# Optimization experiments

Hardware: AMD Instinct MI355X
Metric: run time of the kernel (lower is better)

Reference implementation:

```python
import jax, jax.numpy as jnp
import numpy as np

B, T, D, F, E, TOPK = 4, 2048, 1024, 2752, 8, 2


def setup_inputs() -> dict:
    key = jax.random.key(0)
    k1, k2, k3, k4 = jax.random.split(key, 4)
    x = jax.random.normal(k1, (B, T, D), dtype=jnp.float32)
    # Expert params, torch Linear(bias=False) stored as [in, out] for x @ W
    W13 = jax.random.normal(k2, (E, D, 2 * F), dtype=jnp.float32) * 0.02  # gate+up packed
    W2 = jax.random.normal(k3, (E, F, D), dtype=jnp.float32) * 0.02       # down proj
    Wr = jax.random.normal(k4, (D, E), dtype=jnp.float32) * 0.02          # router
    return {"x": x, "W13": W13, "W2": W2, "Wr": Wr}


def reference(x, W13, W2, Wr):
    b, t, d = x.shape
    xf = x.reshape(-1, d)                       # [N, D]
    n = xf.shape[0]
    logits = xf @ Wr                            # [N, E]
    probs = jax.nn.softmax(logits, axis=-1)
    top_probs, top_idx = jax.lax.top_k(probs, TOPK)  # [N, K]
    top_probs = top_probs / top_probs.sum(axis=-1, keepdims=True)
    # combine weights: cw[n, e] = sum_k top_probs[n, k] * (top_idx[n, k] == e)
    cw = jnp.zeros((n, E), dtype=xf.dtype).at[jnp.arange(n)[:, None], top_idx].add(top_probs)
    out = jnp.zeros_like(xf)
    for e in range(E):  # small fixed expert loop; tokens with cw==0 contribute nothing
        x13 = xf @ W13[e]                       # [N, 2F]
        x1, x3 = jnp.split(x13, 2, axis=-1)
        h = jax.nn.silu(x1) * x3                # SwiGLU
        out = out + cw[:, e:e + 1] * (h @ W2[e])
    return out.reshape(b, t, d)
```

## Files before the change

kernel.cpp:

```cpp
#include <hip/hip_runtime.h>
#include <stdint.h>

#define NTOK 8192
#define DDIM 1024
#define FDIM 2752
#define NEXP 8
#define DF2  5504
#define NSLOT 16384

typedef __attribute__((ext_vector_type(8))) short bf16x8;
typedef __attribute__((ext_vector_type(4))) float f32x4;
typedef __attribute__((ext_vector_type(4))) unsigned short u16x4;
typedef __attribute__((ext_vector_type(8))) unsigned short u16x8;

constexpr size_t XB_OFF   = 0;
constexpr size_t XB_SZ    = (size_t)NTOK * DDIM * 2;
constexpr size_t W13T_OFF = XB_OFF + XB_SZ;
constexpr size_t W13T_SZ  = (size_t)NEXP * DF2 * DDIM * 2;
constexpr size_t W2T_OFF  = W13T_OFF + W13T_SZ;
constexpr size_t W2T_SZ   = (size_t)NEXP * DDIM * FDIM * 2;
constexpr size_t H_OFF    = W2T_OFF + W2T_SZ;
constexpr size_t H_SZ     = (size_t)NSLOT * FDIM * 2;
constexpr size_t ST_OFF   = H_OFF + H_SZ;
constexpr size_t SW_OFF   = ST_OFF + (size_t)NSLOT * 4;
constexpr size_t TTI_OFF  = SW_OFF + (size_t)NSLOT * 4;
constexpr size_t TTW_OFF  = TTI_OFF + (size_t)NTOK * 8;
constexpr size_t META_OFF = TTW_OFF + (size_t)NTOK * 8;

__device__ __forceinline__ unsigned short f2bf(float f) {
  unsigned u = __float_as_uint(f);
  u += 0x7FFFu + ((u >> 16) & 1u);
  return (unsigned short)(u >> 16);
}

__device__ __forceinline__ void gl_lds16(const void* g, void* l) {
  __builtin_amdgcn_global_load_lds(
      (const __attribute__((address_space(1))) unsigned int*)g,
      (__attribute__((address_space(3))) unsigned int*)l, 16, 0, 0);
}

__global__ void cvt_x_k(const float* __restrict__ x, unsigned short* __restrict__ xb) {
  int i = blockIdx.x * 256 + threadIdx.x;
  float4 v = ((const float4*)x)[i];
  u16x4 o;
  o[0] = f2bf(v.x); o[1] = f2bf(v.y); o[2] = f2bf(v.z); o[3] = f2bf(v.w);
  ((u16x4*)xb)[i] = o;
}

__global__ void tcvt_k(const float* __restrict__ src, unsigned short* __restrict__ dst,
                       int R, int C) {
  __shared__ unsigned short tile[64][65];
  long base = (long)blockIdx.z * R * C;
  src += base; dst += base;
  int r0 = blockIdx.y * 64, c0 = blockIdx.x * 64;
  int t = threadIdx.x;
  int rr = t >> 4, cc = (t & 15) * 4;
  for (int i = 0; i < 4; ++i) {
    float4 v = *(const float4*)&src[(long)(r0 + rr + i * 16) * C + c0 + cc];
    tile[rr + i * 16][cc + 0] = f2bf(v.x);
    tile[rr + i * 16][cc + 1] = f2bf(v.y);
    tile[rr + i * 16][cc + 2] = f2bf(v.z);
    tile[rr + i * 16][cc + 3] = f2bf(v.w);
  }
  __syncthreads();
  int dr = t >> 2, sg = (t & 3) * 16;
  u16x8 o0, o1;
  for (int i = 0; i < 8; ++i) { o0[i] = tile[sg + i][dr]; o1[i] = tile[sg + 8 + i][dr]; }
  unsigned short* dp = &dst[(long)(c0 + dr) * R + r0 + sg];
  *(u16x8*)dp = o0;
  *(u16x8*)(dp + 8) = o1;
}

__global__ void router_k(const float* __restrict__ x, const float* __restrict__ Wr,
                         int* __restrict__ meta, int2* __restrict__ tt_i,
                         float2* __restrict__ tt_w) {
  int lane = threadIdx.x & 63;
  int tok = blockIdx.x * 4 + (threadIdx.x >> 6);
  float acc[8];
#pragma unroll
  for (int e = 0; e < 8; ++e) acc[e] = 0.f;
  const float4* xr = (const float4*)(x + (long)tok * DDIM);
#pragma unroll
  for (int it = 0; it < 4; ++it) {
    float4 v = xr[it * 64 + lane];
    int d = (it * 64 + lane) * 4;
    float xv[4] = {v.x, v.y, v.z, v.w};
#pragma unroll
    for (int j = 0; j < 4; ++j) {
      const float4* wr = (const float4*)(Wr + (long)(d + j) * NEXP);
      float4 wa = wr[0], wb = wr[1];
      acc[0] += xv[j] * wa.x; acc[1] += xv[j] * wa.y;
      acc[2] += xv[j] * wa.z; acc[3] += xv[j] * wa.w;
      acc[4] += xv[j] * wb.x; acc[5] += xv[j] * wb.y;
      acc[6] += xv[j] * wb.z; acc[7] += xv[j] * wb.w;
    }
  }
#pragma unroll
  for (int e = 0; e < 8; ++e)
    for (int off = 32; off; off >>= 1) acc[e] += __shfl_xor(acc[e], off, 64);
  if (lane == 0) {
    float m = acc[0];
    for (int e = 1; e < 8; ++e) m = fmaxf(m, acc[e]);
    float p[8];
    for (int e = 0; e < 8; ++e) p[e] = __expf(acc[e] - m);
    int e0 = 0;
    for (int e = 1; e < 8; ++e) if (p[e] > p[e0]) e0 = e;
    int e1 = -1;
    for (int e = 0; e < 8; ++e) { if (e == e0) continue; if (e1 < 0 || p[e] > p[e1]) e1 = e; }
    float s = p[e0] + p[e1];
    atomicAdd(&meta[e0], 1);
    atomicAdd(&meta[e1], 1);
    tt_i[tok] = make_int2(e0, e1);
    tt_w[tok] = make_float2(p[e0] / s, p[e1] / s);
  }
}

__global__ void offsets_k(int* meta) {
  int run = 0;
  for (int e = 0; e < NEXP; ++e) { meta[16 + e] = run; run += meta[e]; }
}

__global__ void scatter_k(const int2* __restrict__ tt_i, const float2* __restrict__ tt_w,
                          int* __restrict__ meta, int* __restrict__ slot_tok,
                          float* __restrict__ slot_w) {
  int n = blockIdx.x * 256 + threadIdx.x;
  int2 ei = tt_i[n];
  float2 wv = tt_w[n];
  int p0 = atomicAdd(&meta[8 + ei.x], 1);
  int s0 = meta[16 + ei.x] + p0;
  slot_tok[s0] = n; slot_w[s0] = wv.x;
  int p1 = atomicAdd(&meta[8 + ei.y], 1);
  int s1 = meta[16 + ei.y] + p1;
  slot_tok[s1] = n; slot_w[s1] = wv.y;
}

__global__ __launch_bounds__(256) void gemm1_k(
    const unsigned short* __restrict__ xb, const unsigned short* __restrict__ w13t,
    const int* __restrict__ meta, const int* __restrict__ slot_tok,
    unsigned short* __restrict__ h) {
  int e = blockIdx.z;
  int n_e = meta[e];
  int m0 = blockIdx.y * 128;
  if (m0 >= n_e) return;
  int base = meta[16 + e];
  int c0 = blockIdx.x * 64;
  const unsigned short* wB = w13t + (long)e * DF2 * DDIM;

  __shared__ unsigned short Al[128 * 32];
  __shared__ unsigned short B1l[64 * 32];
  __shared__ unsigned short B2l[64 * 32];

  int t = threadIdx.x;
  int lane = t & 63, w = t >> 6;
  int wm = w & 1, wn = w >> 1;
  int ar0 = t >> 2, ac = (t & 3) * 8;

  int tokA0 = slot_tok[base + min(m0 + ar0, n_e - 1)];
  int tokA1 = slot_tok[base + min(m0 + 64 + ar0, n_e - 1)];
  const unsigned short* gA0 = xb + (long)tokA0 * DDIM + ac;
  const unsigned short* gA1 = xb + (long)tokA1 * DDIM + ac;
  const unsigned short* gB1 = wB + (long)(c0 + ar0) * DDIM + ac;
  const unsigned short* gB2 = gB1 + (long)FDIM * DDIM;

  unsigned short* lA0 = &Al[t * 8];
  unsigned short* lA1 = &Al[(t + 256) * 8];
  unsigned short* lB1 = &B1l[t * 8];
  unsigned short* lB2 = &B2l[t * 8];

  f32x4 accg[4][2], accu[4][2];
#pragma unroll
  for (int mi = 0; mi < 4; ++mi)
#pragma unroll
    for (int ni = 0; ni < 2; ++ni) {
      accg[mi][ni] = (f32x4){0.f, 0.f, 0.f, 0.f};
      accu[mi][ni] = (f32x4){0.f, 0.f, 0.f, 0.f};
    }

  for (int k0 = 0; k0 < DDIM; k0 += 32) {
    gl_lds16(gA0 + k0, lA0);
    gl_lds16(gA1 + k0, lA1);
    gl_lds16(gB1 + k0, lB1);
    gl_lds16(gB2 + k0, lB2);
    __syncthreads();
    int q8 = (lane >> 4) * 8;
    bf16x8 a[4], b1[2], b2[2];
#pragma unroll
    for (int mi = 0; mi < 4; ++mi)
      a[mi] = *(const bf16x8*)&Al[(wm * 64 + mi * 16 + (lane & 15)) * 32 + q8];
#pragma unroll
    for (int ni = 0; ni < 2; ++ni) {
      b1[ni] = *(const bf16x8*)&B1l[(wn * 32 + ni * 16 + (lane & 15)) * 32 + q8];
      b2[ni] = *(const bf16x8*)&B2l[(wn * 32 + ni * 16 + (lane & 15)) * 32 + q8];
    }
#pragma unroll
    for (int mi = 0; mi < 4; ++mi)
#pragma unroll
      for (int ni = 0; ni < 2; ++ni) {
        accg[mi][ni] = __builtin_amdgcn_mfma_f32_16x16x32_bf16(a[mi], b1[ni], accg[mi][ni], 0, 0, 0);
        accu[mi][ni] = __builtin_amdgcn_mfma_f32_16x16x32_bf16(a[mi], b2[ni], accu[mi][ni], 0, 0, 0);
      }
    __syncthreads();
  }
  int quad = lane >> 4;
  int col0 = c0 + wn * 32 + (lane & 15);
#pragma unroll
  for (int mi = 0; mi < 4; ++mi)
#pragma unroll
    for (int r = 0; r < 4; ++r) {
      int m = m0 + wm * 64 + mi * 16 + quad * 4 + r;
      if (m < n_e) {
        unsigned short* hp = &h[(long)(base + m) * FDIM + col0];
#pragma unroll
        for (int ni = 0; ni < 2; ++ni) {
          float g = accg[mi][ni][r], u = accu[mi][ni][r];
          float hv = (g / (1.f + __expf(-g))) * u;
          hp[ni * 16] = f2bf(hv);
        }
      }
    }
}

__global__ __launch_bounds__(256) void gemm2_k(
    const unsigned short* __restrict__ h, const unsigned short* __restrict__ w2t,
    const int* __restrict__ meta, const int* __restrict__ slot_tok,
    const float* __restrict__ slot_w, float* __restrict__ out) {
  int e = blockIdx.z;
  int n_e = meta[e];
  int m0 = blockIdx.y * 128;
  if (m0 >= n_e) return;
  int base = meta[16 + e];
  int n0 = blockIdx.x * 128;
  const unsigned short* wB = w2t + (long)e * DDIM * FDIM;

  __shared__ unsigned short Al[128 * 32];
  __shared__ unsigned short Bl[128 * 32];

  int t = threadIdx.x;
  int lane = t & 63, w = t >> 6;
  int wm = w & 1, wn = w >> 1;
  int ar0 = t >> 2, ac = (t & 3) * 8;

  int rA0 = base + min(m0 + ar0, n_e - 1);
  int rA1 = base + min(m0 + 64 + ar0, n_e - 1);
  const unsigned short* gA0 = h + (long)rA0 * FDIM + ac;
  const unsigned short* gA1 = h + (long)rA1 * FDIM + ac;
  const unsigned short* gB0 = wB + (long)(n0 + ar0) * FDIM + ac;
  const unsigned short* gB1 = gB0 + (long)64 * FDIM;

  unsigned short* lA0 = &Al[t * 8];
  unsigned short* lA1 = &Al[(t + 256) * 8];
  unsigned short* lB0 = &Bl[t * 8];
  unsigned short* lB1 = &Bl[(t + 256) * 8];

  f32x4 acc[4][4];
#pragma unroll
  for (int mi = 0; mi < 4; ++mi)
#pragma unroll
    for (int ni = 0; ni < 4; ++ni) acc[mi][ni] = (f32x4){0.f, 0.f, 0.f, 0.f};

  for (int k0 = 0; k0 < FDIM; k0 += 32) {
    gl_lds16(gA0 + k0, lA0);
    gl_lds16(gA1 + k0, lA1);
    gl_lds16(gB0 + k0, lB0);
    gl_lds16(gB1 + k0, lB1);
    __syncthreads();
    int q8 = (lane >> 4) * 8;
    bf16x8 a[4], b[4];
#pragma unroll
    for (int mi = 0; mi < 4; ++mi)
      a[mi] = *(const bf16x8*)&Al[(wm * 64 + mi * 16 + (lane & 15)) * 32 + q8];
#pragma unroll
    for (int ni = 0; ni < 4; ++ni)
      b[ni] = *(const bf16x8*)&Bl[(wn * 64 + ni * 16 + (lane & 15)) * 32 + q8];
#pragma unroll
    for (int mi = 0; mi < 4; ++mi)
#pragma unroll
      for (int ni = 0; ni < 4; ++ni)
        acc[mi][ni] = __builtin_amdgcn_mfma_f32_16x16x32_bf16(a[mi], b[ni], acc[mi][ni], 0, 0, 0);
    __syncthreads();
  }
  int quad = lane >> 4;
#pragma unroll
  for (int mi = 0; mi < 4; ++mi)
#pragma unroll
    for (int r = 0; r < 4; ++r) {
      int m = m0 + wm * 64 + mi * 16 + quad * 4 + r;
      if (m < n_e) {
        int tok = slot_tok[base + m];
        float wgt = slot_w[base + m];
        float* op = out + (long)tok * DDIM + n0 + wn * 64 + (lane & 15);
#pragma unroll
        for (int ni = 0; ni < 4; ++ni) atomicAdd(op + ni * 16, wgt * acc[mi][ni][r]);
      }
    }
}

extern "C" void kernel_launch(void* const* d_in, const int* in_sizes, int n_in,
                              void* d_out, int out_size, void* d_ws, size_t ws_size,
                              hipStream_t stream) {
  const float* x   = (const float*)d_in[0];
  const float* W13 = (const float*)d_in[1];
  const float* W2  = (const float*)d_in[2];
  const float* Wr  = (const float*)d_in[3];
  float* out = (float*)d_out;
  char* ws = (char*)d_ws;

  unsigned short* xb   = (unsigned short*)(ws + XB_OFF);
  unsigned short* w13t = (unsigned short*)(ws + W13T_OFF);
  unsigned short* w2t  = (unsigned short*)(ws + W2T_OFF);
  unsigned short* hbuf = (unsigned short*)(ws + H_OFF);
  int*    slot_tok = (int*)(ws + ST_OFF);
  float*  slot_w   = (float*)(ws + SW_OFF);
  int2*   tt_i     = (int2*)(ws + TTI_OFF);
  float2* tt_w     = (float2*)(ws + TTW_OFF);
  int*    meta     = (int*)(ws + META_OFF);

  hipMemsetAsync(d_out, 0, (size_t)NTOK * DDIM * sizeof(float), stream);
  hipMemsetAsync(meta, 0, 128, stream);

  cvt_x_k<<<NTOK * DDIM / 4 / 256, 256, 0, stream>>>(x, xb);
  tcvt_k<<<dim3(DF2 / 64, DDIM / 64, NEXP), 256, 0, stream>>>(W13, w13t, DDIM, DF2);
  tcvt_k<<<dim3(DDIM / 64, FDIM / 64, NEXP), 256, 0, stream>>>(W2, w2t, FDIM, DDIM);
  router_k<<<NTOK / 4, 256, 0, stream>>>(x, Wr, meta, tt_i, tt_w);
  offsets_k<<<1, 1, 0, stream>>>(meta);
  scatter_k<<<NTOK / 256, 256, 0, stream>>>(tt_i, tt_w, meta, slot_tok, slot_w);
  gemm1_k<<<dim3(FDIM / 64, NTOK / 128, NEXP), 256, 0, stream>>>(xb, w13t, meta, slot_tok, hbuf);
  gemm2_k<<<dim3(DDIM / 128, NTOK / 128, NEXP), 256, 0, stream>>>(hbuf, w2t, meta, slot_tok, slot_w, out);
}
```

Measured before the change: 1.109 ms.

## Double-buffer LDS in both expert GEMMs and replace atomic scatter with combine pass

Both grouped GEMMs now double-buffer their LDS tiles. The next K-slice is issued with global_load_lds before the current one is consumed, using explicit vmcnt waits and barriers so load latency overlaps MFMA work. The down-projection no longer atomically adds into the output. It writes weighted per-slot rows to a scratch buffer placed over the W13 workspace, and a new combine kernel sums each token's two slots. This removes atomics and the output memset, at the cost of an extra 64MB write and read pass and one more launch.

```diff
diff --git a/kernel.cpp b/kernel.cpp
--- a/kernel.cpp
+++ b/kernel.cpp
@@ -26,6 +26,7 @@
 constexpr size_t TTI_OFF  = SW_OFF + (size_t)NSLOT * 4;
 constexpr size_t TTW_OFF  = TTI_OFF + (size_t)NTOK * 8;
 constexpr size_t META_OFF = TTW_OFF + (size_t)NTOK * 8;
+constexpr size_t TS_OFF   = META_OFF + 256;
 
 __device__ __forceinline__ unsigned short f2bf(float f) {
   unsigned u = __float_as_uint(f);
@@ -38,6 +39,11 @@
       (const __attribute__((address_space(1))) unsigned int*)g,
       (__attribute__((address_space(3))) unsigned int*)l, 16, 0, 0);
 }
+
+#define WAIT_VM4 asm volatile("s_waitcnt vmcnt(4)" ::: "memory")
+#define WAIT_VM0 asm volatile("s_waitcnt vmcnt(0)" ::: "memory")
+#define WAIT_LGKM0 asm volatile("s_waitcnt lgkmcnt(0)" ::: "memory")
+#define BAR() __builtin_amdgcn_s_barrier()
 
 __global__ void cvt_x_k(const float* __restrict__ x, unsigned short* __restrict__ xb) {
   int i = blockIdx.x * 256 + threadIdx.x;
@@ -122,7 +128,7 @@
 
 __global__ void scatter_k(const int2* __restrict__ tt_i, const float2* __restrict__ tt_w,
                           int* __restrict__ meta, int* __restrict__ slot_tok,
-                          float* __restrict__ slot_w) {
+                          float* __restrict__ slot_w, int2* __restrict__ tok_slot) {
   int n = blockIdx.x * 256 + threadIdx.x;
   int2 ei = tt_i[n];
   float2 wv = tt_w[n];
@@ -132,6 +138,7 @@
   int p1 = atomicAdd(&meta[8 + ei.y], 1);
   int s1 = meta[16 + ei.y] + p1;
   slot_tok[s1] = n; slot_w[s1] = wv.y;
+  tok_slot[n] = make_int2(s0, s1);
 }
 
 __global__ __launch_bounds__(256) void gemm1_k(
@@ -146,9 +153,9 @@
   int c0 = blockIdx.x * 64;
   const unsigned short* wB = w13t + (long)e * DF2 * DDIM;
 
-  __shared__ unsigned short Al[128 * 32];
-  __shared__ unsigned short B1l[64 * 32];
-  __shared__ unsigned short B2l[64 * 32];
+  __shared__ unsigned short Al[2][128 * 32];
+  __shared__ unsigned short B1l[2][64 * 32];
+  __shared__ unsigned short B2l[2][64 * 32];
 
   int t = threadIdx.x;
   int lane = t & 63, w = t >> 6;
@@ -162,11 +169,6 @@
   const unsigned short* gB1 = wB + (long)(c0 + ar0) * DDIM + ac;
   const unsigned short* gB2 = gB1 + (long)FDIM * DDIM;
 
-  unsigned short* lA0 = &Al[t * 8];
-  unsigned short* lA1 = &Al[(t + 256) * 8];
-  unsigned short* lB1 = &B1l[t * 8];
-  unsigned short* lB2 = &B2l[t * 8];
-
   f32x4 accg[4][2], accu[4][2];
 #pragma unroll
   for (int mi = 0; mi < 4; ++mi)
@@ -176,31 +178,60 @@
       accu[mi][ni] = (f32x4){0.f, 0.f, 0.f, 0.f};
     }
 
-  for (int k0 = 0; k0 < DDIM; k0 += 32) {
-    gl_lds16(gA0 + k0, lA0);
-    gl_lds16(gA1 + k0, lA1);
-    gl_lds16(gB1 + k0, lB1);
-    gl_lds16(gB2 + k0, lB2);
-    __syncthreads();
-    int q8 = (lane >> 4) * 8;
-    bf16x8 a[4], b1[2], b2[2];
-#pragma unroll
-    for (int mi = 0; mi < 4; ++mi)
-      a[mi] = *(const bf16x8*)&Al[(wm * 64 + mi * 16 + (lane & 15)) * 32 + q8];
-#pragma unroll
-    for (int ni = 0; ni < 2; ++ni) {
-      b1[ni] = *(const bf16x8*)&B1l[(wn * 32 + ni * 16 + (lane & 15)) * 32 + q8];
-      b2[ni] = *(const bf16x8*)&B2l[(wn * 32 + ni * 16 + (lane & 15)) * 32 + q8];
-    }
-#pragma unroll
-    for (int mi = 0; mi < 4; ++mi)
-#pragma unroll
-      for (int ni = 0; ni < 2; ++ni) {
-        accg[mi][ni] = __builtin_amdgcn_mfma_f32_16x16x32_bf16(a[mi], b1[ni], accg[mi][ni], 0, 0, 0);
-        accu[mi][ni] = __builtin_amdgcn_mfma_f32_16x16x32_bf16(a[mi], b2[ni], accu[mi][ni], 0, 0, 0);
-      }
-    __syncthreads();
-  }
+  int q8 = (lane >> 4) * 8;
+  int arow = lane & 15;
+  bf16x8 a[4], b1[2], b2[2];
+
+#define G1_STAGE(bb, k0)                                      \
+  do {                                                        \
+    gl_lds16(gA0 + (k0), &Al[bb][(size_t)t * 8]);             \
+    gl_lds16(gA1 + (k0), &Al[bb][(size_t)(t + 256) * 8]);     \
+    gl_lds16(gB1 + (k0), &B1l[bb][(size_t)t * 8]);            \
+    gl_lds16(gB2 + (k0), &B2l[bb][(size_t)t * 8]);            \
+  } while (0)
+
+#define G1_FRAGS(bb)                                                          \
+  do {                                                                        \
+    const unsigned short* As = Al[bb];                                        \
+    const unsigned short* B1s = B1l[bb];                                      \
+    const unsigned short* B2s = B2l[bb];                                      \
+    _Pragma("unroll")                                                         \
+    for (int mi = 0; mi < 4; ++mi)                                            \
+      a[mi] = *(const bf16x8*)&As[(wm * 64 + mi * 16 + arow) * 32 + q8];      \
+    _Pragma("unroll")                                                         \
+    for (int ni = 0; ni < 2; ++ni) {                                          \
+      b1[ni] = *(const bf16x8*)&B1s[(wn * 32 + ni * 16 + arow) * 32 + q8];    \
+      b2[ni] = *(const bf16x8*)&B2s[(wn * 32 + ni * 16 + arow) * 32 + q8];    \
+    }                                                                         \
+  } while (0)
+
+#define G1_MFMA()                                                                                    \
+  _Pragma("unroll")                                                                                  \
+  for (int mi = 0; mi < 4; ++mi)                                                                     \
+    _Pragma("unroll")                                                                                \
+    for (int ni = 0; ni < 2; ++ni) {                                                                 \
+      accg[mi][ni] = __builtin_amdgcn_mfma_f32_16x16x32_bf16(a[mi], b1[ni], accg[mi][ni], 0, 0, 0);  \
+      accu[mi][ni] = __builtin_amdgcn_mfma_f32_16x16x32_bf16(a[mi], b2[ni], accu[mi][ni], 0, 0, 0);  \
+    }
+
+  G1_STAGE(0, 0);
+  int cur = 0;
+#pragma unroll 1
+  for (int k = 1; k < DDIM / 32; ++k) {
+    G1_STAGE(cur ^ 1, k * 32);
+    WAIT_VM4;
+    BAR();
+    G1_FRAGS(cur);
+    WAIT_LGKM0;
+    BAR();
+    G1_MFMA();
+    cur ^= 1;
+  }
+  WAIT_VM0;
+  BAR();
+  G1_FRAGS(cur);
+  G1_MFMA();
+
   int quad = lane >> 4;
   int col0 = c0 + wn * 32 + (lane & 15);
 #pragma unroll
@@ -222,8 +253,8 @@
 
 __global__ __launch_bounds__(256) void gemm2_k(
     const unsigned short* __restrict__ h, const unsigned short* __restrict__ w2t,
-    const int* __restrict__ meta, const int* __restrict__ slot_tok,
-    const float* __restrict__ slot_w, float* __restrict__ out) {
+    const int* __restrict__ meta, const float* __restrict__ slot_w,
+    float* __restrict__ y) {
   int e = blockIdx.z;
   int n_e = meta[e];
   int m0 = blockIdx.y * 128;
@@ -232,8 +263,8 @@
   int n0 = blockIdx.x * 128;
   const unsigned short* wB = w2t + (long)e * DDIM * FDIM;
 
-  __shared__ unsigned short Al[128 * 32];
-  __shared__ unsigned short Bl[128 * 32];
+  __shared__ unsigned short Al[2][128 * 32];
+  __shared__ unsigned short Bl[2][128 * 32];
 
   int t = threadIdx.x;
   int lane = t & 63, w = t >> 6;
@@ -247,38 +278,61 @@
   const unsigned short* gB0 = wB + (long)(n0 + ar0) * FDIM + ac;
   const unsigned short* gB1 = gB0 + (long)64 * FDIM;
 
-  unsigned short* lA0 = &Al[t * 8];
-  unsigned short* lA1 = &Al[(t + 256) * 8];
-  unsigned short* lB0 = &Bl[t * 8];
-  unsigned short* lB1 = &Bl[(t + 256) * 8];
-
   f32x4 acc[4][4];
 #pragma unroll
   for (int mi = 0; mi < 4; ++mi)
 #pragma unroll
     for (int ni = 0; ni < 4; ++ni) acc[mi][ni] = (f32x4){0.f, 0.f, 0.f, 0.f};
 
-  for (int k0 = 0; k0 < FDIM; k0 += 32) {
-    gl_lds16(gA0 + k0, lA0);
-    gl_lds16(gA1 + k0, lA1);
-    gl_lds16(gB0 + k0, lB0);
-    gl_lds16(gB1 + k0, lB1);
-    __syncthreads();
-    int q8 = (lane >> 4) * 8;
-    bf16x8 a[4], b[4];
-#pragma unroll
-    for (int mi = 0; mi < 4; ++mi)
-      a[mi] = *(const bf16x8*)&Al[(wm * 64 + mi * 16 + (lane & 15)) * 32 + q8];
-#pragma unroll
-    for (int ni = 0; ni < 4; ++ni)
-      b[ni] = *(const bf16x8*)&Bl[(wn * 64 + ni * 16 + (lane & 15)) * 32 + q8];
-#pragma unroll
-    for (int mi = 0; mi < 4; ++mi)
-#pragma unroll
-      for (int ni = 0; ni < 4; ++ni)
-        acc[mi][ni] = __builtin_amdgcn_mfma_f32_16x16x32_bf16(a[mi], b[ni], acc[mi][ni], 0, 0, 0);
-    __syncthreads();
-  }
+  int q8 = (lane >> 4) * 8;
+  int arow = lane & 15;
+  bf16x8 a[4], b[4];
+
+#define G2_STAGE(bb, k0)                                      \
+  do {                                                        \
+    gl_lds16(gA0 + (k0), &Al[bb][(size_t)t * 8]);             \
+    gl_lds16(gA1 + (k0), &Al[bb][(size_t)(t + 256) * 8]);     \
+    gl_lds16(gB0 + (k0), &Bl[bb][(size_t)t * 8]);             \
+    gl_lds16(gB1 + (k0), &Bl[bb][(size_t)(t + 256) * 8]);     \
+  } while (0)
+
+#define G2_FRAGS(bb)                                                        \
+  do {                                                                      \
+    const unsigned short* As = Al[bb];                                      \
+    const unsigned short* Bs = Bl[bb];                                      \
+    _Pragma("unroll")                                                       \
+    for (int mi = 0; mi < 4; ++mi)                                          \
+      a[mi] = *(const bf16x8*)&As[(wm * 64 + mi * 16 + arow) * 32 + q8];    \
+    _Pragma("unroll")                                                       \
+    for (int ni = 0; ni < 4; ++ni)                                          \
+      b[ni] = *(const bf16x8*)&Bs[(wn * 64 + ni * 16 + arow) * 32 + q8];    \
+  } while (0)
+
+#define G2_MFMA()                                                                                \
+  _Pragma("unroll")                                                                              \
+  for (int mi = 0; mi < 4; ++mi)                                                                 \
+    _Pragma("unroll")                                                                            \
+    for (int ni = 0; ni < 4; ++ni)                                                               \
+      acc[mi][ni] = __builtin_amdgcn_mfma_f32_16x16x32_bf16(a[mi], b[ni], acc[mi][ni], 0, 0, 0);
+
+  G2_STAGE(0, 0);
+  int cur = 0;
+#pragma unroll 1
+  for (int k = 1; k < FDIM / 32; ++k) {
+    G2_STAGE(cur ^ 1, k * 32);
+    WAIT_VM4;
+    BAR();
+    G2_FRAGS(cur);
+    WAIT_LGKM0;
+    BAR();
+    G2_MFMA();
+    cur ^= 1;
+  }
+  WAIT_VM0;
+  BAR();
+  G2_FRAGS(cur);
+  G2_MFMA();
+
   int quad = lane >> 4;
 #pragma unroll
   for (int mi = 0; mi < 4; ++mi)
@@ -286,13 +340,27 @@
     for (int r = 0; r < 4; ++r) {
       int m = m0 + wm * 64 + mi * 16 + quad * 4 + r;
       if (m < n_e) {
-        int tok = slot_tok[base + m];
         float wgt = slot_w[base + m];
-        float* op = out + (long)tok * DDIM + n0 + wn * 64 + (lane & 15);
-#pragma unroll
-        for (int ni = 0; ni < 4; ++ni) atomicAdd(op + ni * 16, wgt * acc[mi][ni][r]);
+        float* yp = y + (long)(base + m) * DDIM + n0 + wn * 64 + (lane & 15);
+#pragma unroll
+        for (int ni = 0; ni < 4; ++ni) yp[ni * 16] = wgt * acc[mi][ni][r];
       }
     }
+}
+
+__global__ void combine_k(const float* __restrict__ y, const int2* __restrict__ tok_slot,
+                          float* __restrict__ out) {
+  int tok = blockIdx.x * 4 + (threadIdx.x >> 6);
+  int lane = threadIdx.x & 63;
+  int2 s = tok_slot[tok];
+  const float4* y0 = (const float4*)(y + (long)s.x * DDIM);
+  const float4* y1 = (const float4*)(y + (long)s.y * DDIM);
+  float4* o = (float4*)(out + (long)tok * DDIM);
+#pragma unroll
+  for (int i = 0; i < 4; ++i) {
+    float4 u = y0[i * 64 + lane], v = y1[i * 64 + lane];
+    o[i * 64 + lane] = make_float4(u.x + v.x, u.y + v.y, u.z + v.z, u.w + v.w);
+  }
 }
 
 extern "C" void kernel_launch(void* const* d_in, const int* in_sizes, int n_in,
@@ -314,8 +382,9 @@
   int2*   tt_i     = (int2*)(ws + TTI_OFF);
   float2* tt_w     = (float2*)(ws + TTW_OFF);
   int*    meta     = (int*)(ws + META_OFF);
-
-  hipMemsetAsync(d_out, 0, (size_t)NTOK * DDIM * sizeof(float), stream);
+  int2*   tok_slot = (int2*)(ws + TS_OFF);
+  float*  ybuf     = (float*)(ws + W13T_OFF);
+
   hipMemsetAsync(meta, 0, 128, stream);
 
   cvt_x_k<<<NTOK * DDIM / 4 / 256, 256, 0, stream>>>(x, xb);
@@ -323,7 +392,8 @@
   tcvt_k<<<dim3(DDIM / 64, FDIM / 64, NEXP), 256, 0, stream>>>(W2, w2t, FDIM, DDIM);
   router_k<<<NTOK / 4, 256, 0, stream>>>(x, Wr, meta, tt_i, tt_w);
   offsets_k<<<1, 1, 0, stream>>>(meta);
-  scatter_k<<<NTOK / 256, 256, 0, stream>>>(tt_i, tt_w, meta, slot_tok, slot_w);
+  scatter_k<<<NTOK / 256, 256, 0, stream>>>(tt_i, tt_w, meta, slot_tok, slot_w, tok_slot);
   gemm1_k<<<dim3(FDIM / 64, NTOK / 128, NEXP), 256, 0, stream>>>(xb, w13t, meta, slot_tok, hbuf);
-  gemm2_k<<<dim3(DDIM / 128, NTOK / 128, NEXP), 256, 0, stream>>>(hbuf, w2t, meta, slot_tok, slot_w, out);
-}
+  gemm2_k<<<dim3(DDIM / 128, NTOK / 128, NEXP), 256, 0, stream>>>(hbuf, w2t, meta, slot_w, ybuf);
+  combine_k<<<NTOK / 4, 256, 0, stream>>>(ybuf, tok_slot, out);
+}
```

Result: no change. 1.122 ms (+1.2%).

## Rewrite expert GEMMs with 256x256 pipelined tiles and atomic-free combine

Applied to the files above, without the earlier changes.

Both expert GEMMs move from 128-row tiles with 256 threads and a single LDS buffer to 256x256 tiles (gate and up rows packed together in gemm1) with 512 threads. They double-buffer LDS with swizzled global-to-LDS loads, manual vmcnt gating, split barriers and s_setprio around the MFMA bursts. gemm2 now writes weighted per-slot rows to a scratch buffer that reuses the W13 workspace, and a new combine kernel sums each token's two slots. This removes the output memset and the float atomics. The cost is larger LDS use, which limits occupancy, plus an extra pass over a 64MB intermediate.

```diff
diff --git a/kernel.cpp b/kernel.cpp
--- a/kernel.cpp
+++ b/kernel.cpp
@@ -7,6 +7,8 @@
 #define NEXP 8
 #define DF2  5504
 #define NSLOT 16384
+#define NT1 16
+#define NT2 43
 
 typedef __attribute__((ext_vector_type(8))) short bf16x8;
 typedef __attribute__((ext_vector_type(4))) float f32x4;
@@ -26,6 +28,7 @@
 constexpr size_t TTI_OFF  = SW_OFF + (size_t)NSLOT * 4;
 constexpr size_t TTW_OFF  = TTI_OFF + (size_t)NTOK * 8;
 constexpr size_t META_OFF = TTW_OFF + (size_t)NTOK * 8;
+constexpr size_t TS_OFF   = META_OFF + 256;
 
 __device__ __forceinline__ unsigned short f2bf(float f) {
   unsigned u = __float_as_uint(f);
@@ -38,6 +41,21 @@
       (const __attribute__((address_space(1))) unsigned int*)g,
       (__attribute__((address_space(3))) unsigned int*)l, 16, 0, 0);
 }
+
+#define BARF()  do { asm volatile("" ::: "memory"); __builtin_amdgcn_s_barrier(); asm volatile("" ::: "memory"); } while (0)
+#define LGKM0   asm volatile("s_waitcnt lgkmcnt(0)" ::: "memory")
+#define GATE6   asm volatile("s_waitcnt vmcnt(6)" ::: "memory")
+#define GATE4   asm volatile("s_waitcnt vmcnt(4)" ::: "memory")
+#define VM0     asm volatile("s_waitcnt vmcnt(0)" ::: "memory")
+#define PRIO1   __builtin_amdgcn_s_setprio(1)
+#define PRIO0   __builtin_amdgcn_s_setprio(0)
+#define MFMA16(aa, bb, cc) cc = __builtin_amdgcn_mfma_f32_16x16x32_bf16(aa, bb, cc, 0, 0, 0)
+
+#define STG(dstbase, parr, koff)                        \
+  do {                                                  \
+    gl_lds16(parr[0] + (koff), (dstbase) + sdst);       \
+    gl_lds16(parr[1] + (koff), (dstbase) + sdst + 512); \
+  } while (0)
 
 __global__ void cvt_x_k(const float* __restrict__ x, unsigned short* __restrict__ xb) {
   int i = blockIdx.x * 256 + threadIdx.x;
@@ -122,7 +140,7 @@
 
 __global__ void scatter_k(const int2* __restrict__ tt_i, const float2* __restrict__ tt_w,
                           int* __restrict__ meta, int* __restrict__ slot_tok,
-                          float* __restrict__ slot_w) {
+                          float* __restrict__ slot_w, int2* __restrict__ tok_slot) {
   int n = blockIdx.x * 256 + threadIdx.x;
   int2 ei = tt_i[n];
   float2 wv = tt_w[n];
@@ -132,167 +150,279 @@
   int p1 = atomicAdd(&meta[8 + ei.y], 1);
   int s1 = meta[16 + ei.y] + p1;
   slot_tok[s1] = n; slot_w[s1] = wv.y;
-}
-
-__global__ __launch_bounds__(256) void gemm1_k(
+  tok_slot[n] = make_int2(s0, s1);
+}
+
+__global__ __launch_bounds__(512, 2) void gemm1_k(
     const unsigned short* __restrict__ xb, const unsigned short* __restrict__ w13t,
     const int* __restrict__ meta, const int* __restrict__ slot_tok,
     unsigned short* __restrict__ h) {
   int e = blockIdx.z;
   int n_e = meta[e];
-  int m0 = blockIdx.y * 128;
+  int m0 = blockIdx.y * 256;
   if (m0 >= n_e) return;
   int base = meta[16 + e];
-  int c0 = blockIdx.x * 64;
+  int c0 = blockIdx.x * 128;
   const unsigned short* wB = w13t + (long)e * DF2 * DDIM;
 
-  __shared__ unsigned short Al[128 * 32];
-  __shared__ unsigned short B1l[64 * 32];
-  __shared__ unsigned short B2l[64 * 32];
+  __shared__ unsigned short Ab[2][2][8192];
+  __shared__ unsigned short Bb[2][2][8192];
 
   int t = threadIdx.x;
   int lane = t & 63, w = t >> 6;
-  int wm = w & 1, wn = w >> 1;
-  int ar0 = t >> 2, ac = (t & 3) * 8;
-
-  int tokA0 = slot_tok[base + min(m0 + ar0, n_e - 1)];
-  int tokA1 = slot_tok[base + min(m0 + 64 + ar0, n_e - 1)];
-  const unsigned short* gA0 = xb + (long)tokA0 * DDIM + ac;
-  const unsigned short* gA1 = xb + (long)tokA1 * DDIM + ac;
-  const unsigned short* gB1 = wB + (long)(c0 + ar0) * DDIM + ac;
-  const unsigned short* gB2 = gB1 + (long)FDIM * DDIM;
-
-  unsigned short* lA0 = &Al[t * 8];
-  unsigned short* lA1 = &Al[(t + 256) * 8];
-  unsigned short* lB1 = &B1l[t * 8];
-  unsigned short* lB2 = &B2l[t * 8];
-
-  f32x4 accg[4][2], accu[4][2];
-#pragma unroll
-  for (int mi = 0; mi < 4; ++mi)
-#pragma unroll
-    for (int ni = 0; ni < 2; ++ni) {
-      accg[mi][ni] = (f32x4){0.f, 0.f, 0.f, 0.f};
-      accu[mi][ni] = (f32x4){0.f, 0.f, 0.f, 0.f};
+  int wm = w >> 2, wn = w & 3;
+  int fr = lane & 15;
+
+  int rj = w * 16 + (lane >> 3);
+  int kc = ((lane & 7) ^ ((lane >> 4) & 2)) * 8;
+  int sdst = w * 1024 + lane * 8;
+
+  const unsigned short* pA[2][2];
+  const unsigned short* pB[2][2];
+#pragma unroll
+  for (int hh = 0; hh < 2; ++hh)
+#pragma unroll
+    for (int j = 0; j < 2; ++j) {
+      int tr = hh * 128 + rj + j * 8;
+      int tok = slot_tok[base + min(m0 + tr, n_e - 1)];
+      pA[hh][j] = xb + (long)tok * DDIM + kc;
+      int wr = (tr < 128) ? min(c0 + tr, FDIM - 1) : FDIM + min(c0 + tr - 128, FDIM - 1);
+      pB[hh][j] = wB + (long)wr * DDIM + kc;
     }
 
-  for (int k0 = 0; k0 < DDIM; k0 += 32) {
-    gl_lds16(gA0 + k0, lA0);
-    gl_lds16(gA1 + k0, lA1);
-    gl_lds16(gB1 + k0, lB1);
-    gl_lds16(gB2 + k0, lB2);
-    __syncthreads();
-    int q8 = (lane >> 4) * 8;
-    bf16x8 a[4], b1[2], b2[2];
-#pragma unroll
-    for (int mi = 0; mi < 4; ++mi)
-      a[mi] = *(const bf16x8*)&Al[(wm * 64 + mi * 16 + (lane & 15)) * 32 + q8];
-#pragma unroll
-    for (int ni = 0; ni < 2; ++ni) {
-      b1[ni] = *(const bf16x8*)&B1l[(wn * 32 + ni * 16 + (lane & 15)) * 32 + q8];
-      b2[ni] = *(const bf16x8*)&B2l[(wn * 32 + ni * 16 + (lane & 15)) * 32 + q8];
-    }
-#pragma unroll
-    for (int mi = 0; mi < 4; ++mi)
-#pragma unroll
-      for (int ni = 0; ni < 2; ++ni) {
-        accg[mi][ni] = __builtin_amdgcn_mfma_f32_16x16x32_bf16(a[mi], b1[ni], accg[mi][ni], 0, 0, 0);
-        accu[mi][ni] = __builtin_amdgcn_mfma_f32_16x16x32_bf16(a[mi], b2[ni], accu[mi][ni], 0, 0, 0);
-      }
-    __syncthreads();
-  }
+  int qp = ((lane >> 4) ^ ((lane >> 2) & 1) * 2) * 8;
+  int abase = fr * 64 + qp;
+  int bbase = wn * 2048 + fr * 64 + qp;
+
+  f32x4 acc[8][4];
+#pragma unroll
+  for (int mi = 0; mi < 8; ++mi)
+#pragma unroll
+    for (int n = 0; n < 4; ++n) acc[mi][n] = (f32x4){0.f, 0.f, 0.f, 0.f};
+  bf16x8 a[8], b0, b1;
+
+  STG(&Ab[0][0][0], pA[0], 0);
+  STG(&Ab[0][1][0], pA[1], 0);
+  STG(&Bb[0][0][0], pB[0], 0);
+  STG(&Bb[0][1][0], pB[1], 0);
+  STG(&Bb[1][0][0], pB[0], (1 < NT1) ? 64 : 0);
+  GATE4;
+  BARF();
+
+#pragma unroll 1
+  for (int U = 0; U < NT1; ++U) {
+    int cur = U & 1, nxt = cur ^ 1;
+    const unsigned short* Ac = &Ab[cur][wm][0];
+    const unsigned short* B0c = &Bb[cur][0][0];
+    const unsigned short* B1c = &Bb[cur][1][0];
+    int k1 = ((U + 1) < NT1) ? (U + 1) * 64 : 0;
+    int k2 = ((U + 2) < NT1) ? (U + 2) * 64 : 0;
+#pragma unroll
+    for (int mi = 0; mi < 8; ++mi) a[mi] = *(const bf16x8*)&Ac[mi * 1024 + abase];
+    b0 = *(const bf16x8*)&B0c[bbase];
+    b1 = *(const bf16x8*)&B0c[1024 + bbase];
+    STG(&Ab[nxt][0][0], pA[0], k1);
+    BARF(); LGKM0;
+    PRIO1;
+#pragma unroll
+    for (int mi = 0; mi < 8; ++mi) { MFMA16(a[mi], b0, acc[mi][0]); MFMA16(a[mi], b1, acc[mi][1]); }
+    PRIO0;
+    GATE4;
+    BARF();
+    b0 = *(const bf16x8*)&B1c[bbase];
+    b1 = *(const bf16x8*)&B1c[1024 + bbase];
+    STG(&Ab[nxt][1][0], pA[1], k1);
+    BARF(); LGKM0;
+    PRIO1;
+#pragma unroll
+    for (int mi = 0; mi < 8; ++mi) { MFMA16(a[mi], b0, acc[mi][2]); MFMA16(a[mi], b1, acc[mi][3]); }
+    PRIO0;
+    BARF();
+#pragma unroll
+    for (int mi = 0; mi < 8; ++mi) a[mi] = *(const bf16x8*)&Ac[mi * 1024 + 32 + abase];
+    b0 = *(const bf16x8*)&B0c[32 + bbase];
+    b1 = *(const bf16x8*)&B0c[1024 + 32 + bbase];
+    STG(&Bb[nxt][1][0], pB[1], k1);
+    BARF(); LGKM0;
+    PRIO1;
+#pragma unroll
+    for (int mi = 0; mi < 8; ++mi) { MFMA16(a[mi], b0, acc[mi][0]); MFMA16(a[mi], b1, acc[mi][1]); }
+    PRIO0;
+    GATE6;
+    BARF();
+    b0 = *(const bf16x8*)&B1c[32 + bbase];
+    b1 = *(const bf16x8*)&B1c[1024 + 32 + bbase];
+    STG(&Bb[cur][0][0], pB[0], k2);
+    BARF(); LGKM0;
+    PRIO1;
+#pragma unroll
+    for (int mi = 0; mi < 8; ++mi) { MFMA16(a[mi], b0, acc[mi][2]); MFMA16(a[mi], b1, acc[mi][3]); }
+    PRIO0;
+    GATE4;
+    BARF();
+  }
+  VM0;
+
   int quad = lane >> 4;
-  int col0 = c0 + wn * 32 + (lane & 15);
-#pragma unroll
-  for (int mi = 0; mi < 4; ++mi)
+#pragma unroll
+  for (int mi = 0; mi < 8; ++mi)
 #pragma unroll
     for (int r = 0; r < 4; ++r) {
-      int m = m0 + wm * 64 + mi * 16 + quad * 4 + r;
+      int m = m0 + wm * 128 + mi * 16 + quad * 4 + r;
       if (m < n_e) {
-        unsigned short* hp = &h[(long)(base + m) * FDIM + col0];
-#pragma unroll
-        for (int ni = 0; ni < 2; ++ni) {
-          float g = accg[mi][ni][r], u = accu[mi][ni][r];
-          float hv = (g / (1.f + __expf(-g))) * u;
-          hp[ni * 16] = f2bf(hv);
+        unsigned short* hp = &h[(long)(base + m) * FDIM];
+#pragma unroll
+        for (int n = 0; n < 2; ++n) {
+          int col = c0 + wn * 32 + n * 16 + fr;
+          if (col < FDIM) {
+            float g = acc[mi][n][r], u = acc[mi][n + 2][r];
+            hp[col] = f2bf((g / (1.f + __expf(-g))) * u);
+          }
         }
       }
     }
 }
 
-__global__ __launch_bounds__(256) void gemm2_k(
-    const unsigned short* __restrict__ h, const unsigned short* __restrict__ w2t,
-    const int* __restrict__ meta, const int* __restrict__ slot_tok,
-    const float* __restrict__ slot_w, float* __restrict__ out) {
+__global__ __launch_bounds__(512, 2) void gemm2_k(
+    const unsigned short* __restrict__ hb, const unsigned short* __restrict__ w2t,
+    const int* __restrict__ meta, const float* __restrict__ slot_w,
+    float* __restrict__ y) {
   int e = blockIdx.z;
   int n_e = meta[e];
-  int m0 = blockIdx.y * 128;
+  int m0 = blockIdx.y * 256;
   if (m0 >= n_e) return;
   int base = meta[16 + e];
-  int n0 = blockIdx.x * 128;
+  int c0 = blockIdx.x * 256;
   const unsigned short* wB = w2t + (long)e * DDIM * FDIM;
 
-  __shared__ unsigned short Al[128 * 32];
-  __shared__ unsigned short Bl[128 * 32];
+  __shared__ unsigned short Ab[2][2][8192];
+  __shared__ unsigned short Bb[2][2][8192];
 
   int t = threadIdx.x;
   int lane = t & 63, w = t >> 6;
-  int wm = w & 1, wn = w >> 1;
-  int ar0 = t >> 2, ac = (t & 3) * 8;
-
-  int rA0 = base + min(m0 + ar0, n_e - 1);
-  int rA1 = base + min(m0 + 64 + ar0, n_e - 1);
-  const unsigned short* gA0 = h + (long)rA0 * FDIM + ac;
-  const unsigned short* gA1 = h + (long)rA1 * FDIM + ac;
-  const unsigned short* gB0 = wB + (long)(n0 + ar0) * FDIM + ac;
-  const unsigned short* gB1 = gB0 + (long)64 * FDIM;
-
-  unsigned short* lA0 = &Al[t * 8];
-  unsigned short* lA1 = &Al[(t + 256) * 8];
-  unsigned short* lB0 = &Bl[t * 8];
-  unsigned short* lB1 = &Bl[(t + 256) * 8];
-
-  f32x4 acc[4][4];
-#pragma unroll
-  for (int mi = 0; mi < 4; ++mi)
-#pragma unroll
-    for (int ni = 0; ni < 4; ++ni) acc[mi][ni] = (f32x4){0.f, 0.f, 0.f, 0.f};
-
-  for (int k0 = 0; k0 < FDIM; k0 += 32) {
-    gl_lds16(gA0 + k0, lA0);
-    gl_lds16(gA1 + k0, lA1);
-    gl_lds16(gB0 + k0, lB0);
-    gl_lds16(gB1 + k0, lB1);
-    __syncthreads();
-    int q8 = (lane >> 4) * 8;
-    bf16x8 a[4], b[4];
-#pragma unroll
-    for (int mi = 0; mi < 4; ++mi)
-      a[mi] = *(const bf16x8*)&Al[(wm * 64 + mi * 16 + (lane & 15)) * 32 + q8];
-#pragma unroll
-    for (int ni = 0; ni < 4; ++ni)
-      b[ni] = *(const bf16x8*)&Bl[(wn * 64 + ni * 16 + (lane & 15)) * 32 + q8];
-#pragma unroll
-    for (int mi = 0; mi < 4; ++mi)
-#pragma unroll
-      for (int ni = 0; ni < 4; ++ni)
-        acc[mi][ni] = __builtin_amdgcn_mfma_f32_16x16x32_bf16(a[mi], b[ni], acc[mi][ni], 0, 0, 0);
-    __syncthreads();
-  }
+  int wm = w >> 2, wn = w & 3;
+  int fr = lane & 15;
+
+  int rj = w * 16 + (lane >> 3);
+  int kc = ((lane & 7) ^ ((lane >> 4) & 2)) * 8;
+  int sdst = w * 1024 + lane * 8;
+
+  const unsigned short* pA[2][2];
+  const unsigned short* pB[2][2];
+#pragma unroll
+  for (int hh = 0; hh < 2; ++hh)
+#pragma unroll
+    for (int j = 0; j < 2; ++j) {
+      int tr = hh * 128 + rj + j * 8;
+      int srow = base + min(m0 + tr, n_e - 1);
+      pA[hh][j] = hb + (long)srow * FDIM + kc;
+      pB[hh][j] = wB + (long)(c0 + tr) * FDIM + kc;
+    }
+
+  int qp = ((lane >> 4) ^ ((lane >> 2) & 1) * 2) * 8;
+  int abase = fr * 64 + qp;
+  int bbase = wn * 2048 + fr * 64 + qp;
+
+  f32x4 acc[8][4];
+#pragma unroll
+  for (int mi = 0; mi < 8; ++mi)
+#pragma unroll
+    for (int n = 0; n < 4; ++n) acc[mi][n] = (f32x4){0.f, 0.f, 0.f, 0.f};
+  bf16x8 a[8], b0, b1;
+
+  STG(&Ab[0][0][0], pA[0], 0);
+  STG(&Ab[0][1][0], pA[1], 0);
+  STG(&Bb[0][0][0], pB[0], 0);
+  STG(&Bb[0][1][0], pB[1], 0);
+  STG(&Bb[1][0][0], pB[0], (1 < NT2) ? 64 : 0);
+  GATE4;
+  BARF();
+
+#pragma unroll 1
+  for (int U = 0; U < NT2; ++U) {
+    int cur = U & 1, nxt = cur ^ 1;
+    const unsigned short* Ac = &Ab[cur][wm][0];
+    const unsigned short* B0c = &Bb[cur][0][0];
+    const unsigned short* B1c = &Bb[cur][1][0];
+    int k1 = ((U + 1) < NT2) ? (U + 1) * 64 : 0;
+    int k2 = ((U + 2) < NT2) ? (U + 2) * 64 : 0;
+#pragma unroll
+    for (int mi = 0; mi < 8; ++mi) a[mi] = *(const bf16x8*)&Ac[mi * 1024 + abase];
+    b0 = *(const bf16x8*)&B0c[bbase];
+    b1 = *(const bf16x8*)&B0c[1024 + bbase];
+    STG(&Ab[nxt][0][0], pA[0], k1);
+    BARF(); LGKM0;
+    PRIO1;
+#pragma unroll
+    for (int mi = 0; mi < 8; ++mi) { MFMA16(a[mi], b0, acc[mi][0]); MFMA16(a[mi], b1, acc[mi][1]); }
+    PRIO0;
+    GATE4;
+    BARF();
+    b0 = *(const bf16x8*)&B1c[bbase];
+    b1 = *(const bf16x8*)&B1c[1024 + bbase];
+    STG(&Ab[nxt][1][0], pA[1], k1);
+    BARF(); LGKM0;
+    PRIO1;
+#pragma unroll
+    for (int mi = 0; mi < 8; ++mi) { MFMA16(a[mi], b0, acc[mi][2]); MFMA16(a[mi], b1, acc[mi][3]); }
+    PRIO0;
+    BARF();
+#pragma unroll
+    for (int mi = 0; mi < 8; ++mi) a[mi] = *(const bf16x8*)&Ac[mi * 1024 + 32 + abase];
+    b0 = *(const bf16x8*)&B0c[32 + bbase];
+    b1 = *(const bf16x8*)&B0c[1024 + 32 + bbase];
+    STG(&Bb[nxt][1][0], pB[1], k1);
+    BARF(); LGKM0;
+    PRIO1;
+#pragma unroll
+    for (int mi = 0; mi < 8; ++mi) { MFMA16(a[mi], b0, acc[mi][0]); MFMA16(a[mi], b1, acc[mi][1]); }
+    PRIO0;
+    GATE6;
+    BARF();
+    b0 = *(const bf16x8*)&B1c[32 + bbase];
+    b1 = *(const bf16x8*)&B1c[1024 + 32 + bbase];
+    STG(&Bb[cur][0][0], pB[0], k2);
+    BARF(); LGKM0;
+    PRIO1;
+#pragma unroll
+    for (int mi = 0; mi < 8; ++mi) { MFMA16(a[mi], b0, acc[mi][2]); MFMA16(a[mi], b1, acc[mi][3]); }
+    PRIO0;
+    GATE4;
+    BARF();
+  }
+  VM0;
+
   int quad = lane >> 4;
 #pragma unroll
-  for (int mi = 0; mi < 4; ++mi)
+  for (int mi = 0; mi < 8; ++mi)
 #pragma unroll
     for (int r = 0; r < 4; ++r) {
-      int m = m0 + wm * 64 + mi * 16 + quad * 4 + r;
+      int m = m0 + wm * 128 + mi * 16 + quad * 4 + r;
       if (m < n_e) {
-        int tok = slot_tok[base + m];
         float wgt = slot_w[base + m];
-        float* op = out + (long)tok * DDIM + n0 + wn * 64 + (lane & 15);
-#pragma unroll
-        for (int ni = 0; ni < 4; ++ni) atomicAdd(op + ni * 16, wgt * acc[mi][ni][r]);
+        float* yp = y + (long)(base + m) * DDIM;
+#pragma unroll
+        for (int n = 0; n < 4; ++n) {
+          int col = c0 + (n >> 1) * 128 + wn * 32 + (n & 1) * 16 + fr;
+          yp[col] = wgt * acc[mi][n][r];
+        }
       }
     }
+}
+
+__global__ void combine_k(const float* __restrict__ y, const int2* __restrict__ tok_slot,
+                          float* __restrict__ out) {
+  int tok = blockIdx.x * 4 + (threadIdx.x >> 6);
+  int lane = threadIdx.x & 63;
+  int2 s = tok_slot[tok];
+  const float4* y0 = (const float4*)(y + (long)s.x * DDIM);
+  const float4* y1 = (const float4*)(y + (long)s.y * DDIM);
+  float4* o = (float4*)(out + (long)tok * DDIM);
+#pragma unroll
+  for (int i = 0; i < 4; ++i) {
+    float4 u = y0[i * 64 + lane], v = y1[i * 64 + lane];
+    o[i * 64 + lane] = make_float4(u.x + v.x, u.y + v.y, u.z + v.z, u.w + v.w);
+  }
 }
 
 extern "C" void kernel_launch(void* const* d_in, const int* in_sizes, int n_in,
@@ -314,8 +444,9 @@
   int2*   tt_i     = (int2*)(ws + TTI_OFF);
   float2* tt_w     = (float2*)(ws + TTW_OFF);
   int*    meta     = (int*)(ws + META_OFF);
-
-  hipMemsetAsync(d_out, 0, (size_t)NTOK * DDIM * sizeof(float), stream);
+  int2*   tok_slot = (int2*)(ws + TS_OFF);
+  float*  ybuf     = (float*)(ws + W13T_OFF);
+
   hipMemsetAsync(meta, 0, 128, stream);
 
   cvt_x_k<<<NTOK * DDIM / 4 / 256, 256, 0, stream>>>(x, xb);
@@ -323,7 +454,8 @@
   tcvt_k<<<dim3(DDIM / 64, FDIM / 64, NEXP), 256, 0, stream>>>(W2, w2t, FDIM, DDIM);
   router_k<<<NTOK / 4, 256, 0, stream>>>(x, Wr, meta, tt_i, tt_w);
   offsets_k<<<1, 1, 0, stream>>>(meta);
-  scatter_k<<<NTOK / 256, 256, 0, stream>>>(tt_i, tt_w, meta, slot_tok, slot_w);
-  gemm1_k<<<dim3(FDIM / 64, NTOK / 128, NEXP), 256, 0, stream>>>(xb, w13t, meta, slot_tok, hbuf);
-  gemm2_k<<<dim3(DDIM / 128, NTOK / 128, NEXP), 256, 0, stream>>>(hbuf, w2t, meta, slot_tok, slot_w, out);
-}
+  scatter_k<<<NTOK / 256, 256, 0, stream>>>(tt_i, tt_w, meta, slot_tok, slot_w, tok_slot);
+  gemm1_k<<<dim3(FDIM / 128 + 1, NTOK / 256, NEXP), 512, 0, stream>>>(xb, w13t, meta, slot_tok, hbuf);
+  gemm2_k<<<dim3(DDIM / 256, NTOK / 256, NEXP), 512, 0, stream>>>(hbuf, w2t, meta, slot_w, ybuf);
+  combine_k<<<NTOK / 4, 256, 0, stream>>>(ybuf, tok_slot, out);
+}
```

Measured after the change: 1.113 ms. Within noise of the previous version (+0.4%).
